# Kernel tuning notes

Hardware: AMD Instinct MI355X
Metric: run time of the kernel (lower is better)

Reference implementation:

```python
import jax, jax.numpy as jnp
import numpy as np

B, T, H, A, V, L = 4096, 16, 768, 128, 16, 2

def setup_inputs() -> dict:
    key = jax.random.key(0)
    ks = jax.random.split(key, 8)
    s = 0.02
    return {
        "last_hidden": jax.random.normal(ks[0], (B, T, H), jnp.float32),
        "attention_mask": jnp.ones((B, T), jnp.int64),
        "variety_ids": jax.random.randint(ks[1], (B,), 0, V),
        "Wd": jax.random.normal(ks[2], (V, H, A), jnp.float32) * s,  # per-variety down-proj
        "bd": jnp.zeros((V, A), jnp.float32),
        "Wu": jax.random.normal(ks[3], (V, A, H), jnp.float32) * s,  # per-variety up-proj
        "bu": jnp.zeros((V, H), jnp.float32),
        "Wc": jax.random.normal(ks[4], (L, H), jnp.float32) * s,     # classifier
        "bc": jnp.zeros((L,), jnp.float32),
    }

def reference(last_hidden, attention_mask, variety_ids, Wd, bd, Wu, bu, Wc, bc):
    x = last_hidden[:, 0, :]                                   # (B,H) CLS token
    # Dense grouped adapter: run all V bottleneck adapters, then select per example.
    h = jax.nn.gelu(jnp.einsum('bh,vha->bva', x, Wd) + bd[None])   # (B,V,A)
    u = jnp.einsum('bva,vah->bvh', h, Wu) + bu[None]               # (B,V,H)
    sel = u[jnp.arange(x.shape[0]), variety_ids]                   # (B,H) routed output
    adapted = x + sel                                              # residual bottleneck adapter
    # dropout is identity at p=0.0 / eval
    return adapted @ Wc.T + bc                                     # (B,L) logits
```

## Files before the change

### kernel.cpp

```cpp
#include <hip/hip_runtime.h>
#include <hip/hip_bf16.h>

#define BB 4096
#define TT 16
#define HH 768
#define AA 128
#define VV 16
#define LL 2
#define NCHUNK 6
#define MT 16

typedef __attribute__((ext_vector_type(8))) short short8v;
typedef __attribute__((ext_vector_type(4))) float float4v;

#define WS_OFFS 0
#define WS_ROWS 64
#define WS_WUC  4160
#define WS_BUC  8256
#define WS_WDP  8448

__device__ __forceinline__ unsigned short f2bf(float f) {
    __hip_bfloat16 h = __float2bfloat16(f);
    return *reinterpret_cast<unsigned short*>(&h);
}

__device__ __forceinline__ float gelu_tanh(float z) {
    float y = 0.7978845608028654f * (z + 0.044715f * z * z * z);
    y = fminf(fmaxf(y, -15.f), 15.f);
    float e = __expf(2.f * y);
    float th = (e - 1.f) / (e + 1.f);
    return 0.5f * z * (1.f + th);
}

__global__ __launch_bounds__(256) void k_prep(
    const int*   __restrict__ variety_ids,
    const float* __restrict__ Wd,
    const float* __restrict__ Wu,
    const float* __restrict__ bu,
    const float* __restrict__ Wc,
    int* __restrict__ ws_i)
{
    __shared__ __align__(16) unsigned short Wds[128 * 136];
    __shared__ float sp0[256], sp1[256];
    __shared__ int hist[VV], hoff[VV + 1], hcur[VV];

    const int t = threadIdx.x;
    const int bid = blockIdx.x;
    unsigned short* wdp = (unsigned short*)(ws_i + WS_WDP);
    float* Wuc = (float*)(ws_i + WS_WUC);
    float* buc = (float*)(ws_i + WS_BUC);

    if (bid < 96) {
        const int v = bid / NCHUNK, kc = bid % NCHUNK;
        const float* wd = Wd + (size_t)v * HH * AA;
        const int ks0 = kc * 128;
        #pragma unroll
        for (int s = 0; s < 16; ++s) {
            int idx = t + s * 256;
            int hl  = idx >> 5;
            int a4  = idx & 31;
            float4 wv = *(const float4*)(wd + (size_t)(ks0 + hl) * AA + a4 * 4);
            Wds[(a4 * 4 + 0) * 136 + hl] = f2bf(wv.x);
            Wds[(a4 * 4 + 1) * 136 + hl] = f2bf(wv.y);
            Wds[(a4 * 4 + 2) * 136 + hl] = f2bf(wv.z);
            Wds[(a4 * 4 + 3) * 136 + hl] = f2bf(wv.w);
        }
        __syncthreads();
        unsigned short* dst = wdp + (size_t)(v * NCHUNK + kc) * AA * 128;
        #pragma unroll
        for (int s = 0; s < 8; ++s) {
            int G = t + s * 256;
            int a = G >> 4, g = G & 15;
            uint4 w = *(const uint4*)&Wds[a * 136 + g * 8];
            *(uint4*)&dst[a * 128 + g * 8] = w;
        }
    } else if (bid < 224) {
        const int v = (bid - 96) >> 3;
        const int g = (bid - 96) & 7;
        const int a_loc = t >> 4;
        const int q     = t & 15;
        const int a = g * 16 + a_loc;
        const float* wu = Wu + (size_t)v * AA * HH + (size_t)a * HH;
        float s0 = 0.f, s1 = 0.f;
        #pragma unroll 4
        for (int h = q * 48; h < q * 48 + 48; h += 4) {
            float4 w  = *(const float4*)&wu[h];
            float4 c0 = *(const float4*)&Wc[h];
            float4 c1 = *(const float4*)&Wc[HH + h];
            s0 += w.x * c0.x + w.y * c0.y + w.z * c0.z + w.w * c0.w;
            s1 += w.x * c1.x + w.y * c1.y + w.z * c1.z + w.w * c1.w;
        }
        sp0[a_loc * 16 + q] = s0;
        sp1[a_loc * 16 + q] = s1;
        __syncthreads();
        if (t < 16) {
            float r0 = 0.f, r1 = 0.f;
            #pragma unroll
            for (int i = 0; i < 16; ++i) { r0 += sp0[t * 16 + i]; r1 += sp1[t * 16 + i]; }
            int aa = g * 16 + t;
            Wuc[(v * AA + aa) * LL + 0] = r0;
            Wuc[(v * AA + aa) * LL + 1] = r1;
        }
    } else if (bid == 224) {
        const int pair = t >> 3, seg = t & 7;
        const int v = pair >> 1, l = pair & 1;
        float s = 0.f;
        const float* bv = bu + (size_t)v * HH;
        for (int h = seg * 96; h < seg * 96 + 96; ++h) s += bv[h] * Wc[l * HH + h];
        sp0[t] = s;
        __syncthreads();
        if (t < 32) {
            float r = 0.f;
            #pragma unroll
            for (int i = 0; i < 8; ++i) r += sp0[t * 8 + i];
            buc[t] = r;
        }
    } else {
        if (t < VV) hist[t] = 0;
        __syncthreads();
        for (int b = t; b < BB; b += 256) atomicAdd(&hist[variety_ids[b]], 1);
        __syncthreads();
        if (t == 0) {
            int s = 0;
            for (int i = 0; i < VV; ++i) { hoff[i] = s; s += hist[i]; }
            hoff[VV] = s;
            for (int i = 0; i <= VV; ++i) ws_i[WS_OFFS + i] = hoff[i];
        }
        __syncthreads();
        if (t < VV) hcur[t] = hoff[t];
        __syncthreads();
        for (int b = t; b < BB; b += 256) {
            int v = variety_ids[b];
            int p = atomicAdd(&hcur[v], 1);
            ws_i[WS_ROWS + p] = b;
        }
    }
}

__global__ __launch_bounds__(256) void k_main(
    const float* __restrict__ last_hidden,
    const int*   __restrict__ ws_i,
    const float* __restrict__ bd,
    const float* __restrict__ Wc,
    const float* __restrict__ bc,
    float* __restrict__ out)
{
    __shared__ __align__(16) unsigned short Xs[2][MT * 136];
    __shared__ __align__(16) float p_part[MT * LL * 64];
    __shared__ int srows[MT];
    __shared__ float xc[MT * LL];

    const int* offs = ws_i + WS_OFFS;
    const int* rows = ws_i + WS_ROWS;
    const float* Wuc = (const float*)(ws_i + WS_WUC);
    const float* buc = (const float*)(ws_i + WS_BUC);
    const unsigned short* wdp = (const unsigned short*)(ws_i + WS_WDP);
    const int t = threadIdx.x;

    const int rt = blockIdx.x;
    int v = -1, tloc = 0, cnt = 0, obase = 0, acc_t = 0;
    for (int vv = 0; vv < VV; ++vv) {
        int c  = offs[vv + 1] - offs[vv];
        int nt = (c + MT - 1) / MT;
        if (rt < acc_t + nt) {
            v = vv; tloc = rt - acc_t;
            cnt = c - tloc * MT; if (cnt > MT) cnt = MT;
            obase = offs[vv];
            break;
        }
        acc_t += nt;
    }
    if (v < 0) return;

    if (t < MT) {
        int rr = t < cnt ? t : cnt - 1;
        srows[t] = rows[obase + tloc * MT + rr];
    }
    __syncthreads();

    const int lane = t & 63;
    const int wv_  = t >> 6;
    const int ac0  = wv_ * 32;
    const int m = lane & 15, quad = lane >> 4;
    const int r0 = t >> 5, k4 = t & 31;

    const float* xb0 = last_hidden + (size_t)srows[r0]     * TT * HH + k4 * 4;
    const float* xb1 = last_hidden + (size_t)srows[r0 + 8] * TT * HH + k4 * 4;
    const unsigned short* wdv = wdp + (size_t)v * NCHUNK * AA * 128;
    const unsigned short* bp0 = wdv + (size_t)(ac0 + m)      * 128 + quad * 8;
    const unsigned short* bp1 = wdv + (size_t)(ac0 + 16 + m) * 128 + quad * 8;
    const float* cfp = Wc + (size_t)m * HH + quad * 8;

    float4v acc[2];
    float4v accx;
    acc[0] = (float4v){0.f, 0.f, 0.f, 0.f};
    acc[1] = (float4v){0.f, 0.f, 0.f, 0.f};
    accx   = (float4v){0.f, 0.f, 0.f, 0.f};

    float4 xA = *(const float4*)xb0;
    float4 xB = *(const float4*)xb1;
    short8v Bn[8];
    #pragma unroll
    for (int i = 0; i < 4; ++i) {
        Bn[i]     = *(const short8v*)(bp0 + i * 32);
        Bn[4 + i] = *(const short8v*)(bp1 + i * 32);
    }

    #pragma unroll
    for (int kc = 0; kc < NCHUNK; ++kc) {
        float4 xAc = xA, xBc = xB;
        short8v Bc[8];
        #pragma unroll
        for (int i = 0; i < 8; ++i) Bc[i] = Bn[i];

        if (kc + 1 < NCHUNK) {
            xA = *(const float4*)(xb0 + (kc + 1) * 128);
            xB = *(const float4*)(xb1 + (kc + 1) * 128);
            #pragma unroll
            for (int i = 0; i < 4; ++i) {
                Bn[i]     = *(const short8v*)(bp0 + (size_t)(kc + 1) * AA * 128 + i * 32);
                Bn[4 + i] = *(const short8v*)(bp1 + (size_t)(kc + 1) * AA * 128 + i * 32);
            }
        }

        unsigned short* xs = (unsigned short*)Xs[kc & 1];
        {
            unsigned int q0 = (unsigned)f2bf(xAc.x) | ((unsigned)f2bf(xAc.y) << 16);
            unsigned int q1 = (unsigned)f2bf(xAc.z) | ((unsigned)f2bf(xAc.w) << 16);
            *(uint2*)&xs[r0 * 136 + k4 * 4] = make_uint2(q0, q1);
            q0 = (unsigned)f2bf(xBc.x) | ((unsigned)f2bf(xBc.y) << 16);
            q1 = (unsigned)f2bf(xBc.z) | ((unsigned)f2bf(xBc.w) << 16);
            *(uint2*)&xs[(r0 + 8) * 136 + k4 * 4] = make_uint2(q0, q1);
        }
        __syncthreads();

        float4 cfa[8];
        if (wv_ == 0 && m < LL) {
            #pragma unroll
            for (int i = 0; i < 4; ++i) {
                cfa[2 * i]     = *(const float4*)(cfp + kc * 128 + i * 32);
                cfa[2 * i + 1] = *(const float4*)(cfp + kc * 128 + i * 32 + 4);
            }
        }

        #pragma unroll
        for (int i = 0; i < 4; ++i) {
            short8v af = *(const short8v*)&xs[m * 136 + i * 32 + quad * 8];
            acc[0] = __builtin_amdgcn_mfma_f32_16x16x32_bf16(af, Bc[i],     acc[0], 0, 0, 0);
            acc[1] = __builtin_amdgcn_mfma_f32_16x16x32_bf16(af, Bc[4 + i], acc[1], 0, 0, 0);
            if (wv_ == 0) {
                short8v cf = (short8v){0, 0, 0, 0, 0, 0, 0, 0};
                if (m < LL) {
                    float4 c0 = cfa[2 * i], c1 = cfa[2 * i + 1];
                    cf[0] = (short)f2bf(c0.x); cf[1] = (short)f2bf(c0.y);
                    cf[2] = (short)f2bf(c0.z); cf[3] = (short)f2bf(c0.w);
                    cf[4] = (short)f2bf(c1.x); cf[5] = (short)f2bf(c1.y);
                    cf[6] = (short)f2bf(c1.z); cf[7] = (short)f2bf(c1.w);
                }
                accx = __builtin_amdgcn_mfma_f32_16x16x32_bf16(af, cf, accx, 0, 0, 0);
            }
        }
    }

    {
        float bdv[2], w0v[2], w1v[2];
        #pragma unroll
        for (int j = 0; j < 2; ++j) {
            int a = ac0 + j * 16 + m;
            bdv[j] = bd[v * AA + a];
            w0v[j] = Wuc[(v * AA + a) * LL + 0];
            w1v[j] = Wuc[(v * AA + a) * LL + 1];
        }
        #pragma unroll
        for (int reg = 0; reg < 4; ++reg) {
            int row = quad * 4 + reg;
            float p0 = 0.f, p1 = 0.f;
            #pragma unroll
            for (int j = 0; j < 2; ++j) {
                float h = gelu_tanh(acc[j][reg] + bdv[j]);
                p0 += h * w0v[j];
                p1 += h * w1v[j];
            }
            p_part[(row * LL + 0) * 64 + wv_ * 16 + m] = p0;
            p_part[(row * LL + 1) * 64 + wv_ * 16 + m] = p1;
        }
        if (wv_ == 0 && m < LL) {
            #pragma unroll
            for (int reg = 0; reg < 4; ++reg) {
                int row = quad * 4 + reg;
                xc[row * LL + m] = accx[reg];
            }
        }
    }
    __syncthreads();

    if (t < MT * LL) {
        int row = t >> 1, l = t & 1;
        if (row < cnt) {
            float s = 0.f;
            #pragma unroll
            for (int k = 0; k < 64; ++k) s += p_part[(row * LL + l) * 64 + k];
            int gr = srows[row];
            out[(size_t)gr * LL + l] = s + xc[row * LL + l] + buc[v * LL + l] + bc[l];
        }
    }
}

extern "C" void kernel_launch(void* const* d_in, const int* in_sizes, int n_in,
                              void* d_out, int out_size, void* d_ws, size_t ws_size,
                              hipStream_t stream) {
    const float* last_hidden = (const float*)d_in[0];
    const int*   variety_ids = (const int*)d_in[2];
    const float* Wd = (const float*)d_in[3];
    const float* bd = (const float*)d_in[4];
    const float* Wu = (const float*)d_in[5];
    const float* bu = (const float*)d_in[6];
    const float* Wc = (const float*)d_in[7];
    const float* bc = (const float*)d_in[8];
    float* out = (float*)d_out;

    int* ws_i = (int*)d_ws;

    k_prep<<<226, 256, 0, stream>>>(variety_ids, Wd, Wu, bu, Wc, ws_i);
    k_main<<<271, 256, 0, stream>>>(last_hidden, ws_i, bd, Wc, bc, out);
}
```

Before: 269.1 us.

## Load X directly into MFMA registers and double row tile per block

Result: slower. 280.8 us (+4.4%).

```diff
diff --git a/kernel.cpp b/kernel.cpp
--- a/kernel.cpp
+++ b/kernel.cpp
@@ -8,7 +8,7 @@
 #define VV 16
 #define LL 2
 #define NCHUNK 6
-#define MT 16
+#define MT 32
 
 typedef __attribute__((ext_vector_type(8))) short short8v;
 typedef __attribute__((ext_vector_type(4))) float float4v;
@@ -137,7 +137,7 @@
     }
 }
 
-__global__ __launch_bounds__(256) void k_main(
+__global__ __launch_bounds__(512) void k_main(
     const float* __restrict__ last_hidden,
     const int*   __restrict__ ws_i,
     const float* __restrict__ bd,
@@ -145,7 +145,6 @@
     const float* __restrict__ bc,
     float* __restrict__ out)
 {
-    __shared__ __align__(16) unsigned short Xs[2][MT * 136];
     __shared__ __align__(16) float p_part[MT * LL * 64];
     __shared__ int srows[MT];
     __shared__ float xc[MT * LL];
@@ -179,13 +178,13 @@
     __syncthreads();
 
     const int lane = t & 63;
-    const int wv_  = t >> 6;
-    const int ac0  = wv_ * 32;
+    const int wid  = t >> 6;
+    const int grp  = wid >> 2;
+    const int wq   = wid & 3;
+    const int ac0  = wq * 32;
     const int m = lane & 15, quad = lane >> 4;
-    const int r0 = t >> 5, k4 = t & 31;
-
-    const float* xb0 = last_hidden + (size_t)srows[r0]     * TT * HH + k4 * 4;
-    const float* xb1 = last_hidden + (size_t)srows[r0 + 8] * TT * HH + k4 * 4;
+
+    const float* xb = last_hidden + (size_t)srows[grp * 16 + m] * TT * HH + quad * 8;
     const unsigned short* wdv = wdp + (size_t)v * NCHUNK * AA * 128;
     const unsigned short* bp0 = wdv + (size_t)(ac0 + m)      * 128 + quad * 8;
     const unsigned short* bp1 = wdv + (size_t)(ac0 + 16 + m) * 128 + quad * 8;
@@ -197,45 +196,36 @@
     acc[1] = (float4v){0.f, 0.f, 0.f, 0.f};
     accx   = (float4v){0.f, 0.f, 0.f, 0.f};
 
-    float4 xA = *(const float4*)xb0;
-    float4 xB = *(const float4*)xb1;
+    float4 xn[8];
     short8v Bn[8];
     #pragma unroll
     for (int i = 0; i < 4; ++i) {
+        xn[2 * i]     = *(const float4*)(xb + i * 32);
+        xn[2 * i + 1] = *(const float4*)(xb + i * 32 + 4);
         Bn[i]     = *(const short8v*)(bp0 + i * 32);
         Bn[4 + i] = *(const short8v*)(bp1 + i * 32);
     }
 
     #pragma unroll
     for (int kc = 0; kc < NCHUNK; ++kc) {
-        float4 xAc = xA, xBc = xB;
+        float4 xcur[8];
         short8v Bc[8];
         #pragma unroll
-        for (int i = 0; i < 8; ++i) Bc[i] = Bn[i];
+        for (int i = 0; i < 8; ++i) { xcur[i] = xn[i]; Bc[i] = Bn[i]; }
 
         if (kc + 1 < NCHUNK) {
-            xA = *(const float4*)(xb0 + (kc + 1) * 128);
-            xB = *(const float4*)(xb1 + (kc + 1) * 128);
+            const int base = (kc + 1) * 128;
             #pragma unroll
             for (int i = 0; i < 4; ++i) {
+                xn[2 * i]     = *(const float4*)(xb + base + i * 32);
+                xn[2 * i + 1] = *(const float4*)(xb + base + i * 32 + 4);
                 Bn[i]     = *(const short8v*)(bp0 + (size_t)(kc + 1) * AA * 128 + i * 32);
                 Bn[4 + i] = *(const short8v*)(bp1 + (size_t)(kc + 1) * AA * 128 + i * 32);
             }
         }
 
-        unsigned short* xs = (unsigned short*)Xs[kc & 1];
-        {
-            unsigned int q0 = (unsigned)f2bf(xAc.x) | ((unsigned)f2bf(xAc.y) << 16);
-            unsigned int q1 = (unsigned)f2bf(xAc.z) | ((unsigned)f2bf(xAc.w) << 16);
-            *(uint2*)&xs[r0 * 136 + k4 * 4] = make_uint2(q0, q1);
-            q0 = (unsigned)f2bf(xBc.x) | ((unsigned)f2bf(xBc.y) << 16);
-            q1 = (unsigned)f2bf(xBc.z) | ((unsigned)f2bf(xBc.w) << 16);
-            *(uint2*)&xs[(r0 + 8) * 136 + k4 * 4] = make_uint2(q0, q1);
-        }
-        __syncthreads();
-
         float4 cfa[8];
-        if (wv_ == 0 && m < LL) {
+        if (wq == 0 && m < LL) {
             #pragma unroll
             for (int i = 0; i < 4; ++i) {
                 cfa[2 * i]     = *(const float4*)(cfp + kc * 128 + i * 32);
@@ -245,10 +235,16 @@
 
         #pragma unroll
         for (int i = 0; i < 4; ++i) {
-            short8v af = *(const short8v*)&xs[m * 136 + i * 32 + quad * 8];
+            float4 a0 = xcur[2 * i], a1 = xcur[2 * i + 1];
+            short8v af;
+            af[0] = (short)f2bf(a0.x); af[1] = (short)f2bf(a0.y);
+            af[2] = (short)f2bf(a0.z); af[3] = (short)f2bf(a0.w);
+            af[4] = (short)f2bf(a1.x); af[5] = (short)f2bf(a1.y);
+            af[6] = (short)f2bf(a1.z); af[7] = (short)f2bf(a1.w);
+
             acc[0] = __builtin_amdgcn_mfma_f32_16x16x32_bf16(af, Bc[i],     acc[0], 0, 0, 0);
             acc[1] = __builtin_amdgcn_mfma_f32_16x16x32_bf16(af, Bc[4 + i], acc[1], 0, 0, 0);
-            if (wv_ == 0) {
+            if (wq == 0) {
                 short8v cf = (short8v){0, 0, 0, 0, 0, 0, 0, 0};
                 if (m < LL) {
                     float4 c0 = cfa[2 * i], c1 = cfa[2 * i + 1];
@@ -273,7 +269,7 @@
         }
         #pragma unroll
         for (int reg = 0; reg < 4; ++reg) {
-            int row = quad * 4 + reg;
+            int row = grp * 16 + quad * 4 + reg;
             float p0 = 0.f, p1 = 0.f;
             #pragma unroll
             for (int j = 0; j < 2; ++j) {
@@ -281,13 +277,13 @@
                 p0 += h * w0v[j];
                 p1 += h * w1v[j];
             }
-            p_part[(row * LL + 0) * 64 + wv_ * 16 + m] = p0;
-            p_part[(row * LL + 1) * 64 + wv_ * 16 + m] = p1;
-        }
-        if (wv_ == 0 && m < LL) {
+            p_part[(row * LL + 0) * 64 + wq * 16 + m] = p0;
+            p_part[(row * LL + 1) * 64 + wq * 16 + m] = p1;
+        }
+        if (wq == 0 && m < LL) {
             #pragma unroll
             for (int reg = 0; reg < 4; ++reg) {
-                int row = quad * 4 + reg;
+                int row = grp * 16 + quad * 4 + reg;
                 xc[row * LL + m] = accx[reg];
             }
         }
@@ -322,5 +318,5 @@
     int* ws_i = (int*)d_ws;
 
     k_prep<<<226, 256, 0, stream>>>(variety_ids, Wd, Wu, bu, Wc, ws_i);
-    k_main<<<271, 256, 0, stream>>>(last_hidden, ws_i, bd, Wc, bc, out);
-}
+    k_main<<<144, 512, 0, stream>>>(last_hidden, ws_i, bd, Wc, bc, out);
+}
```
